# Performance work log

Measured on AMD Instinct MI355X. Metric: run time of the kernel, lower is better.

## Reference

```python
import jax, jax.numpy as jnp
import numpy as np

CHUNK = 512  # query-point chunk size; per-chunk intermediate is CHUNK x M x 3


def _min_sqdist(a, b):
    """For each point in a [N,3], min over b [M,3] of squared Euclidean distance.
    Chunked over a to avoid materializing the full NxM matrix (mirrors KDTree's
    avoidance of the dense matrix)."""
    n = a.shape[0]
    a_chunks = a.reshape(n // CHUNK, CHUNK, a.shape[1])

    def body(carry, ac):
        # ac: [CHUNK,3]; d: [CHUNK,M]
        d = jnp.sum((ac[:, None, :] - b[None, :, :]) ** 2, axis=-1)
        return carry, jnp.min(d, axis=1)

    _, mins = jax.lax.scan(body, None, a_chunks)
    return mins.reshape(n)


def setup_inputs() -> dict:
    key = jax.random.key(0)
    k1, k2 = jax.random.split(key)
    gt_points = jax.random.normal(k1, (16384, 3), dtype=jnp.float32)
    gen_points = jax.random.normal(k2, (16384, 3), dtype=jnp.float32)
    return {"gt_points": gt_points, "gen_points": gen_points}


def reference(gt_points, gen_points):
    # KDTree.query returns Euclidean distance; original squares then means,
    # which equals mean of squared nearest-neighbor distances.
    gt_to_gen = jnp.mean(_min_sqdist(gt_points, gen_points))
    gen_to_gt = jnp.mean(_min_sqdist(gen_points, gt_points))
    return gt_to_gen + gen_to_gt
```

## Files before the change

### kernel.cpp

```cpp
#include <hip/hip_runtime.h>
#include <float.h>


#define NPTS 16384
constexpr int QPB   = 64;
constexpr int NBLK  = NPTS / QPB;
constexpr int NFRAG = NPTS / 32;
constexpr int FPW   = NFRAG / 8;
constexpr int SET_SHORTS = NFRAG * 512;

typedef float f32x16 __attribute__((ext_vector_type(16)));
typedef short bf16x8 __attribute__((ext_vector_type(8)));

__device__ inline ushort bf16rne(float f) {
    uint u = __float_as_uint(f);
    u += 0x7fff + ((u >> 16) & 1);
    return (ushort)(u >> 16);
}
__device__ inline float bf2f(ushort h) { return __uint_as_float(((uint)h) << 16); }

__global__ __launch_bounds__(512) void cd_prep(const float* __restrict__ gt,
                                               const float* __restrict__ gen,
                                               short* __restrict__ bt) {
    const int t   = blockIdx.x * 512 + threadIdx.x;
    const int set = t >> 15;
    const int rem = t & 32767;
    const int h   = rem >> 14;
    const int p   = rem & (NPTS - 1);
    const float* __restrict__ src = set ? gen : gt;

    const float x = src[3 * p + 0], y = src[3 * p + 1], z = src[3 * p + 2];
    const ushort hx = bf16rne(x), hy = bf16rne(y), hz = bf16rne(z);
    const ushort lx = bf16rne(x - bf2f(hx));
    const ushort ly = bf16rne(y - bf2f(hy));
    const ushort lz = bf16rne(z - bf2f(hz));
    const float w = fmaf(x, x, fmaf(y, y, z * z));
    const ushort wh = bf16rne(w), wl = bf16rne(w - bf2f(wh));

    bf16x8 v;
    if (h == 0)
        v = (bf16x8){(short)hx, (short)hy, (short)hz, (short)hx,
                     (short)hy, (short)hz, (short)lx, (short)ly};
    else
        v = (bf16x8){(short)lz, (short)lx, (short)ly, (short)lz,
                     (short)wh, (short)wl, (short)0, (short)0};
    *(bf16x8*)(bt + set * SET_SHORTS + (p >> 5) * 512 + (h * 32 + (p & 31)) * 8) = v;
}

__global__ __launch_bounds__(512, 4) void cd_main(const float* __restrict__ gt,
                                                  const float* __restrict__ gen,
                                                  const short* __restrict__ bt,
                                                  float* __restrict__ part) {
    const int dir = blockIdx.y;
    const float* __restrict__ Q = dir ? gen : gt;
    const short* __restrict__ BT = bt + (dir ? 0 : SET_SHORTS);

    __shared__ float wm[8][QPB];

    const int tid  = threadIdx.x;
    const int lane = tid & 63;
    const int wave = __builtin_amdgcn_readfirstlane(tid >> 6);

    const int arow = lane & 31, kg = lane >> 5;
    const int qbase = blockIdx.x * QPB;
    bf16x8 a[2];
    #pragma unroll
    for (int f = 0; f < 2; ++f) {
        const int q = qbase + f * 32 + arow;
        const float x = Q[3 * q + 0], y = Q[3 * q + 1], z = Q[3 * q + 2];
        const float ux = -2.f * x, uy = -2.f * y, uz = -2.f * z;
        const ushort hx = bf16rne(ux), hy = bf16rne(uy), hz = bf16rne(uz);
        const ushort lx = bf16rne(ux - bf2f(hx));
        const ushort ly = bf16rne(uy - bf2f(hy));
        const ushort lz = bf16rne(uz - bf2f(hz));
        if (kg == 0)
            a[f] = (bf16x8){(short)hx, (short)hy, (short)hz, (short)lx,
                            (short)ly, (short)lz, (short)hx, (short)hy};
        else
            a[f] = (bf16x8){(short)hz, (short)lx, (short)ly, (short)lz,
                            (short)0x3f80, (short)0x3f80, (short)0, (short)0};
    }

    f32x16 mm0 = (f32x16)(FLT_MAX), mm1 = (f32x16)(FLT_MAX);
    const f32x16 zc = (f32x16)(0.f);

    const short* rb = BT + (wave * FPW) * 512 + lane * 8;
    for (int f2 = 0; f2 < FPW; f2 += 2) {
        const bf16x8 b0 = *(const bf16x8*)(rb + f2 * 512);
        const bf16x8 b1 = *(const bf16x8*)(rb + (f2 + 1) * 512);
        const f32x16 d00 = __builtin_amdgcn_mfma_f32_32x32x16_bf16(a[0], b0, zc, 0, 0, 0);
        const f32x16 d01 = __builtin_amdgcn_mfma_f32_32x32x16_bf16(a[0], b1, zc, 0, 0, 0);
        #pragma unroll
        for (int i = 0; i < 16; ++i)
            mm0[i] = fminf(fminf(d00[i], d01[i]), mm0[i]);
        const f32x16 d10 = __builtin_amdgcn_mfma_f32_32x32x16_bf16(a[1], b0, zc, 0, 0, 0);
        const f32x16 d11 = __builtin_amdgcn_mfma_f32_32x32x16_bf16(a[1], b1, zc, 0, 0, 0);
        #pragma unroll
        for (int i = 0; i < 16; ++i)
            mm1[i] = fminf(fminf(d10[i], d11[i]), mm1[i]);
    }

    #pragma unroll
    for (int i = 0; i < 16; ++i) {
        float v0 = mm0[i], v1 = mm1[i];
        #pragma unroll
        for (int off = 1; off <= 16; off <<= 1) {
            v0 = fminf(v0, __shfl_xor(v0, off, 64));
            v1 = fminf(v1, __shfl_xor(v1, off, 64));
        }
        const int row = (i & 3) + 8 * (i >> 2) + 4 * kg;
        if ((lane & 31) == 0) {
            wm[wave][row]      = v0;
            wm[wave][32 + row] = v1;
        }
    }
    __syncthreads();

    if (tid < QPB) {
        float v = wm[0][tid];
        #pragma unroll
        for (int w = 1; w < 8; ++w) v = fminf(v, wm[w][tid]);
        const int q = qbase + tid;
        const float x = Q[3 * q + 0], y = Q[3 * q + 1], z = Q[3 * q + 2];
        v += fmaf(x, x, fmaf(y, y, z * z));
        #pragma unroll
        for (int off = 32; off > 0; off >>= 1) v += __shfl_down(v, off, 64);
        if (tid == 0) part[blockIdx.y * NBLK + blockIdx.x] = v;
    }
}

__global__ __launch_bounds__(512) void cd_reduce(const float* __restrict__ part,
                                                 float* __restrict__ out) {
    float v = part[threadIdx.x];
    #pragma unroll
    for (int off = 32; off > 0; off >>= 1) v += __shfl_down(v, off, 64);
    __shared__ float ws[8];
    const int lane = threadIdx.x & 63, w = threadIdx.x >> 6;
    if (lane == 0) ws[w] = v;
    __syncthreads();
    if (threadIdx.x == 0) {
        float s = 0.0f;
        #pragma unroll
        for (int i = 0; i < 8; ++i) s += ws[i];
        out[0] = s * (1.0f / (float)NPTS);
    }
}

extern "C" void kernel_launch(void* const* d_in, const int* in_sizes, int n_in,
                              void* d_out, int out_size, void* d_ws, size_t ws_size,
                              hipStream_t stream) {
    const float* gt  = (const float*)d_in[0];
    const float* gen = (const float*)d_in[1];
    short* bt        = (short*)d_ws;
    float* part      = (float*)((short*)d_ws + 2 * SET_SHORTS);
    float* out       = (float*)d_out;

    cd_prep<<<128, 512, 0, stream>>>(gt, gen, bt);
    dim3 grid(NBLK, 2);
    cd_main<<<grid, 512, 0, stream>>>(gt, gen, bt, part);
    cd_reduce<<<1, 512, 0, stream>>>(part, out);
}
```

Before: 81.71 us.

## Tile reference points into LDS and split work across query and target tiles

```diff
diff --git a/kernel.cpp b/kernel.cpp
--- a/kernel.cpp
+++ b/kernel.cpp
@@ -3,11 +3,13 @@
 
 
 #define NPTS 16384
-constexpr int QPB   = 64;
-constexpr int NBLK  = NPTS / QPB;
+constexpr int QPB   = 512;
+constexpr int NQB   = NPTS / QPB;
 constexpr int NFRAG = NPTS / 32;
-constexpr int FPW   = NFRAG / 8;
-constexpr int SET_SHORTS = NFRAG * 512;
+constexpr int FPC   = 64;
+constexpr int NTC   = NFRAG / FPC;
+constexpr int FRAG_SHORTS = 512;
+constexpr int SET_SHORTS  = NFRAG * FRAG_SHORTS;
 
 typedef float f32x16 __attribute__((ext_vector_type(16)));
 typedef short bf16x8 __attribute__((ext_vector_type(8)));
@@ -21,7 +23,10 @@
 
 __global__ __launch_bounds__(512) void cd_prep(const float* __restrict__ gt,
                                                const float* __restrict__ gen,
-                                               short* __restrict__ bt) {
+                                               short* __restrict__ bt,
+                                               float* __restrict__ out) {
+    if (blockIdx.x == 0 && threadIdx.x == 0) out[0] = 0.0f;
+
     const int t   = blockIdx.x * 512 + threadIdx.x;
     const int set = t >> 15;
     const int rem = t & 32767;
@@ -44,29 +49,38 @@
     else
         v = (bf16x8){(short)lz, (short)lx, (short)ly, (short)lz,
                      (short)wh, (short)wl, (short)0, (short)0};
-    *(bf16x8*)(bt + set * SET_SHORTS + (p >> 5) * 512 + (h * 32 + (p & 31)) * 8) = v;
+    *(bf16x8*)(bt + set * SET_SHORTS + (p >> 5) * FRAG_SHORTS
+               + (h * 32 + (p & 31)) * 8) = v;
 }
 
-__global__ __launch_bounds__(512, 4) void cd_main(const float* __restrict__ gt,
+__global__ __launch_bounds__(512, 2) void cd_main(const float* __restrict__ gt,
                                                   const float* __restrict__ gen,
                                                   const short* __restrict__ bt,
-                                                  float* __restrict__ part) {
-    const int dir = blockIdx.y;
+                                                  float* __restrict__ part2) {
+    const int tc  = blockIdx.y & (NTC - 1);
+    const int dir = blockIdx.y >> 3;
     const float* __restrict__ Q = dir ? gen : gt;
-    const short* __restrict__ BT = bt + (dir ? 0 : SET_SHORTS);
+    const short* __restrict__ BT = bt + (dir ? 0 : SET_SHORTS)
+                                 + tc * FPC * FRAG_SHORTS;
 
-    __shared__ float wm[8][QPB];
+    __shared__ short FRsh[FPC * FRAG_SHORTS];
 
     const int tid  = threadIdx.x;
     const int lane = tid & 63;
     const int wave = __builtin_amdgcn_readfirstlane(tid >> 6);
 
+    #pragma unroll
+    for (int k = 0; k < 8; ++k) {
+        const int idx = k * 512 + tid;
+        ((bf16x8*)FRsh)[idx] = ((const bf16x8*)BT)[idx];
+    }
+
     const int arow = lane & 31, kg = lane >> 5;
-    const int qbase = blockIdx.x * QPB;
+    const int qw = blockIdx.x * QPB + wave * 64;
     bf16x8 a[2];
     #pragma unroll
     for (int f = 0; f < 2; ++f) {
-        const int q = qbase + f * 32 + arow;
+        const int q = qw + f * 32 + arow;
         const float x = Q[3 * q + 0], y = Q[3 * q + 1], z = Q[3 * q + 2];
         const float ux = -2.f * x, uy = -2.f * y, uz = -2.f * z;
         const ushort hx = bf16rne(ux), hy = bf16rne(uy), hz = bf16rne(uz);
@@ -84,10 +98,12 @@
     f32x16 mm0 = (f32x16)(FLT_MAX), mm1 = (f32x16)(FLT_MAX);
     const f32x16 zc = (f32x16)(0.f);
 
-    const short* rb = BT + (wave * FPW) * 512 + lane * 8;
-    for (int f2 = 0; f2 < FPW; f2 += 2) {
-        const bf16x8 b0 = *(const bf16x8*)(rb + f2 * 512);
-        const bf16x8 b1 = *(const bf16x8*)(rb + (f2 + 1) * 512);
+    __syncthreads();
+
+    const short* rb = FRsh + lane * 8;
+    for (int f2 = 0; f2 < FPC; f2 += 2) {
+        const bf16x8 b0 = *(const bf16x8*)(rb + f2 * FRAG_SHORTS);
+        const bf16x8 b1 = *(const bf16x8*)(rb + (f2 + 1) * FRAG_SHORTS);
         const f32x16 d00 = __builtin_amdgcn_mfma_f32_32x32x16_bf16(a[0], b0, zc, 0, 0, 0);
         const f32x16 d01 = __builtin_amdgcn_mfma_f32_32x32x16_bf16(a[0], b1, zc, 0, 0, 0);
         #pragma unroll
@@ -100,6 +116,7 @@
             mm1[i] = fminf(fminf(d10[i], d11[i]), mm1[i]);
     }
 
+    float* pd = part2 + (size_t)blockIdx.y * NPTS + qw;
     #pragma unroll
     for (int i = 0; i < 16; ++i) {
         float v0 = mm0[i], v1 = mm1[i];
@@ -110,28 +127,28 @@
         }
         const int row = (i & 3) + 8 * (i >> 2) + 4 * kg;
         if ((lane & 31) == 0) {
-            wm[wave][row]      = v0;
-            wm[wave][32 + row] = v1;
+            pd[row]      = v0;
+            pd[32 + row] = v1;
         }
-    }
-    __syncthreads();
-
-    if (tid < QPB) {
-        float v = wm[0][tid];
-        #pragma unroll
-        for (int w = 1; w < 8; ++w) v = fminf(v, wm[w][tid]);
-        const int q = qbase + tid;
-        const float x = Q[3 * q + 0], y = Q[3 * q + 1], z = Q[3 * q + 2];
-        v += fmaf(x, x, fmaf(y, y, z * z));
-        #pragma unroll
-        for (int off = 32; off > 0; off >>= 1) v += __shfl_down(v, off, 64);
-        if (tid == 0) part[blockIdx.y * NBLK + blockIdx.x] = v;
     }
 }
 
-__global__ __launch_bounds__(512) void cd_reduce(const float* __restrict__ part,
+__global__ __launch_bounds__(512) void cd_finish(const float* __restrict__ gt,
+                                                 const float* __restrict__ gen,
+                                                 const float* __restrict__ part2,
                                                  float* __restrict__ out) {
-    float v = part[threadIdx.x];
+    const int t   = blockIdx.x * 512 + threadIdx.x;
+    const int dir = t >> 14;
+    const int q   = t & (NPTS - 1);
+    const float* __restrict__ Q = dir ? gen : gt;
+
+    float m = FLT_MAX;
+    #pragma unroll
+    for (int tc = 0; tc < NTC; ++tc)
+        m = fminf(m, part2[(size_t)(dir * NTC + tc) * NPTS + q]);
+    const float x = Q[3 * q + 0], y = Q[3 * q + 1], z = Q[3 * q + 2];
+    float v = m + fmaf(x, x, fmaf(y, y, z * z));
+
     #pragma unroll
     for (int off = 32; off > 0; off >>= 1) v += __shfl_down(v, off, 64);
     __shared__ float ws[8];
@@ -142,7 +159,7 @@
         float s = 0.0f;
         #pragma unroll
         for (int i = 0; i < 8; ++i) s += ws[i];
-        out[0] = s * (1.0f / (float)NPTS);
+        atomicAdd(out, s * (1.0f / (float)NPTS));
     }
 }
 
@@ -152,11 +169,11 @@
     const float* gt  = (const float*)d_in[0];
     const float* gen = (const float*)d_in[1];
     short* bt        = (short*)d_ws;
-    float* part      = (float*)((short*)d_ws + 2 * SET_SHORTS);
+    float* part2     = (float*)((short*)d_ws + 2 * SET_SHORTS);
     float* out       = (float*)d_out;
 
-    cd_prep<<<128, 512, 0, stream>>>(gt, gen, bt);
-    dim3 grid(NBLK, 2);
-    cd_main<<<grid, 512, 0, stream>>>(gt, gen, bt, part);
-    cd_reduce<<<1, 512, 0, stream>>>(part, out);
+    cd_prep<<<128, 512, 0, stream>>>(gt, gen, bt, out);
+    dim3 grid(NQB, NTC * 2);
+    cd_main<<<grid, 512, 0, stream>>>(gt, gen, bt, part2);
+    cd_finish<<<64, 512, 0, stream>>>(gt, gen, part2, out);
 }
```

Measured after the change: 80.26 us. About the same (-1.8%).
